# Optimization experiments

Measured on AMD Instinct MI355X. Metric: run time of the kernel, lower is better.

The kernel has to match this reference:

```python
import jax, jax.numpy as jnp
import numpy as np

RADIUS = 1.3
RES = 128
SH_DEG = 2
N_SH = (SH_DEG + 1) ** 2          # 9 SH basis functions
DATA_DIM = N_SH * 3 + 1           # 28: 27 SH rgb coeffs + 1 sigma
STEP = (2.0 * RADIUS / RES) / 2.0 # half a voxel, as in calc_step_size
N_INTRS = int(np.ceil(np.sqrt(3.0) * 2.0 * RES))  # torch.arange(float) length
N_RAYS = 4096


def sh_basis(d):
    # Real spherical harmonics up to degree 2, svox2/plenoxels convention. d: [B,3]
    x, y, z = d[:, 0], d[:, 1], d[:, 2]
    return jnp.stack([
        0.28209479177387814 * jnp.ones_like(x),
        -0.4886025119029199 * y,
        0.4886025119029199 * z,
        -0.4886025119029199 * x,
        1.0925484305920792 * x * y,
        -1.0925484305920792 * y * z,
        0.31539156525252005 * (2.0 * z * z - x * x - y * y),
        -1.0925484305920792 * x * z,
        0.5462742152960396 * (x * x - y * y),
    ], axis=-1)  # [B, 9]


def trilerp(grid, pts):
    # grid: [C, R, R, R] laid out (D,H,W); pts: [N,3] as (x,y,z) in [-1,1],
    # x indexes W, y indexes H, z indexes D (torch grid_sample convention),
    # align_corners=True, padding_mode='border'. Returns [C, N].
    R = grid.shape[-1]
    c = jnp.clip((pts + 1.0) * 0.5 * (R - 1), 0.0, R - 1)  # border padding
    c0 = jnp.floor(c)
    f = c - c0
    i0 = c0.astype(jnp.int32)
    i1 = jnp.minimum(i0 + 1, R - 1)
    x0, y0, z0 = i0[:, 0], i0[:, 1], i0[:, 2]
    x1, y1, z1 = i1[:, 0], i1[:, 1], i1[:, 2]
    fx, fy, fz = f[:, 0], f[:, 1], f[:, 2]
    g = lambda zi, yi, xi: grid[:, zi, yi, xi]  # [C, N]
    out = (g(z0, y0, x0) * ((1 - fz) * (1 - fy) * (1 - fx)) +
           g(z0, y0, x1) * ((1 - fz) * (1 - fy) * fx) +
           g(z0, y1, x0) * ((1 - fz) * fy * (1 - fx)) +
           g(z0, y1, x1) * ((1 - fz) * fy * fx) +
           g(z1, y0, x0) * (fz * (1 - fy) * (1 - fx)) +
           g(z1, y0, x1) * (fz * (1 - fy) * fx) +
           g(z1, y1, x0) * (fz * fy * (1 - fx)) +
           g(z1, y1, x1) * (fz * fy * fx))
    return out


def setup_inputs() -> dict:
    key = jax.random.key(0)
    k1, k2, k3 = jax.random.split(key, 3)
    rays_o = jax.random.normal(k1, (N_RAYS, 3), jnp.float32) * 0.3  # inside cube
    rd = jax.random.normal(k2, (N_RAYS, 3), jnp.float32)
    rays_d = rd / jnp.linalg.norm(rd, axis=-1, keepdims=True)
    # grid parameter: SH coeffs init 0.1, sigma init 0.01 (as in module) + noise
    base = jnp.concatenate([
        jnp.full((1, DATA_DIM - 1, RES, RES, RES), 0.1, jnp.float32),
        jnp.full((1, 1, RES, RES, RES), 0.01, jnp.float32)], axis=1)
    data = base + 0.01 * jax.random.normal(k3, (1, DATA_DIM, RES, RES, RES), jnp.float32)
    return {"rays_o": rays_o, "rays_d": rays_d, "data": data}


def reference(rays_o, rays_d, data):
    # --- ray/box intersection sampling (no grad in original) ---
    ro = jax.lax.stop_gradient(rays_o)
    rd = jax.lax.stop_gradient(rays_d)
    off_pos = (RADIUS - ro) / rd
    off_neg = (-RADIUS - ro) / rd
    start = jnp.max(jnp.minimum(off_pos, off_neg), axis=-1, keepdims=True)  # [B,1]
    steps = jnp.arange(N_INTRS, dtype=ro.dtype)[None, :]
    intersections = start + steps * STEP          # [B, N_INTRS]
    t = intersections[:, :-1]                     # [B, NI]
    pts = ro[:, None, :] + t[..., None] * rd[:, None, :]  # [B, NI, 3]
    mask = jnp.all((pts > -RADIUS) & (pts < RADIUS), axis=-1)  # [B, NI]
    ptsn = pts / RADIUS
    B, NI = t.shape

    # --- trilinear interpolation of grid at all sample points ---
    interp = trilerp(data[0], ptsn.reshape(-1, 3)).T  # [B*NI, 28]
    sigma = jax.nn.relu(interp[:, -1].reshape(B, NI))
    sigma = jnp.where(mask, sigma, 0.0)  # masked_scatter into zeros

    # --- sigma2alpha: standard volumetric compositing weights ---
    dists = (intersections[:, 1:] - intersections[:, :-1]) \
            * jnp.linalg.norm(rays_d, axis=-1, keepdims=True)  # [B, NI]
    alpha = 1.0 - jnp.exp(-sigma * dists)
    trans = jnp.cumprod(jnp.concatenate(
        [jnp.ones((B, 1), alpha.dtype), 1.0 - alpha + 1e-10], axis=1), axis=1)[:, :-1]
    abs_light = alpha * trans  # [B, NI]

    # --- SH -> rgb per sample ---
    sh_mult = sh_basis(rays_d)  # [B, 9]
    sh = interp[:, :-1].reshape(B, NI, 3, N_SH)
    rgb_pts = jnp.einsum('bk,bnck->bnc', sh_mult, sh)  # [B, NI, 3]
    rgb_pts = jnp.where(mask[..., None], rgb_pts, 0.0)  # masked_scatter

    # --- shrgb2rgb: sigmoid, composite, white background ---
    rgb = jnp.sum(abs_light[..., None] * jax.nn.sigmoid(rgb_pts), axis=1)  # [B,3]
    rgb = rgb + (1.0 - jnp.sum(abs_light, axis=1))[..., None]  # white bkgd
    return rgb
```

## Files before the change

kernel.cpp:

```cpp
#include <hip/hip_runtime.h>
#include <math.h>


typedef _Float16 h8 __attribute__((ext_vector_type(8)));

namespace {
constexpr float kRadius   = 1.3f;
constexpr int   kRes      = 128;
constexpr float kStep     = 2.0f * 1.3f / 128.0f / 2.0f;
constexpr int   kNI       = 443;
constexpr int   kNRays    = 4096;
constexpr int   kChStride = kRes * kRes * kRes;
constexpr int   kCh       = 28;
constexpr int   kVoxPad   = 32;
constexpr size_t kVoxBytes = (size_t)kChStride * kVoxPad * sizeof(_Float16);
constexpr int   kChunks   = 2;
constexpr int   kChunks7  = 7;
}

__global__ __launch_bounds__(256)
void convert_grid(const float* __restrict__ grid, _Float16* __restrict__ vox)
{
    const int v = blockIdx.x * 256 + threadIdx.x;
    h8 o[4];
    #pragma unroll
    for (int c = 0; c < kCh; ++c)
        o[c >> 3][c & 7] = (_Float16)__builtin_nontemporal_load(grid + (size_t)c * kChStride + v);
    o[3][4] = o[3][5] = o[3][6] = o[3][7] = (_Float16)0.f;

    h8* dst = (h8*)(vox + (size_t)v * kVoxPad);
    dst[0] = o[0]; dst[1] = o[1]; dst[2] = o[2]; dst[3] = o[3];
}

struct Sample {
    float alpha;
    float a;
    float rp0, rp1, rp2;
    bool  inb;
};

__device__ __forceinline__ Sample eval_sample(
    int k, float start, float ox, float oy, float oz,
    float dx, float dy, float dz, float dist,
    const float* __restrict__ shm, const _Float16* __restrict__ vox)
{
    Sample s;
    s.alpha = 0.f; s.a = 1.f; s.rp0 = s.rp1 = s.rp2 = 0.f; s.inb = false;
    if (k >= kNI) return s;

    const float t  = start + (float)k * kStep;
    const float px = ox + t*dx;
    const float py = oy + t*dy;
    const float pz = oz + t*dz;
    s.inb = (px > -kRadius) && (px < kRadius) &&
            (py > -kRadius) && (py < kRadius) &&
            (pz > -kRadius) && (pz < kRadius);

    float sig = 0.0f;
    if (s.inb) {
        const float cx = fminf(fmaxf((px*(1.0f/kRadius) + 1.0f)*0.5f*127.0f, 0.0f), 127.0f);
        const float cy = fminf(fmaxf((py*(1.0f/kRadius) + 1.0f)*0.5f*127.0f, 0.0f), 127.0f);
        const float cz = fminf(fmaxf((pz*(1.0f/kRadius) + 1.0f)*0.5f*127.0f, 0.0f), 127.0f);
        const float fx0 = floorf(cx), fy0 = floorf(cy), fz0 = floorf(cz);
        const float fx = cx - fx0, fy = cy - fy0, fz = cz - fz0;
        const int ix0 = (int)fx0, iy0 = (int)fy0, iz0 = (int)fz0;
        const int ix1 = min(ix0 + 1, 127);
        const int iy1 = min(iy0 + 1, 127);
        const int iz1 = min(iz0 + 1, 127);

        const float gx0 = 1.0f - fx, gy0 = 1.0f - fy, gz0 = 1.0f - fz;

        const int offs[8] = {
            iz0*(kRes*kRes) + iy0*kRes + ix0,
            iz0*(kRes*kRes) + iy0*kRes + ix1,
            iz0*(kRes*kRes) + iy1*kRes + ix0,
            iz0*(kRes*kRes) + iy1*kRes + ix1,
            iz1*(kRes*kRes) + iy0*kRes + ix0,
            iz1*(kRes*kRes) + iy0*kRes + ix1,
            iz1*(kRes*kRes) + iy1*kRes + ix0,
            iz1*(kRes*kRes) + iy1*kRes + ix1 };
        const float cw[8] = {
            gz0*gy0*gx0, gz0*gy0*fx, gz0*fy*gx0, gz0*fy*fx,
            fz *gy0*gx0, fz *gy0*fx, fz *fy*gx0, fz *fy*fx };

        #pragma unroll
        for (int cn = 0; cn < 8; ++cn) {
            const h8* vp = (const h8*)(vox + (size_t)offs[cn] * kVoxPad);
            const h8 q0 = vp[0], q1 = vp[1], q2 = vp[2], q3 = vp[3];

            float f[28];
            #pragma unroll
            for (int i = 0; i < 8; ++i) f[i]      = (float)q0[i];
            #pragma unroll
            for (int i = 0; i < 8; ++i) f[8 + i]  = (float)q1[i];
            #pragma unroll
            for (int i = 0; i < 8; ++i) f[16 + i] = (float)q2[i];
            #pragma unroll
            for (int i = 0; i < 4; ++i) f[24 + i] = (float)q3[i];

            float r = 0.f, g = 0.f, b = 0.f;
            #pragma unroll
            for (int j = 0; j < 9; ++j) {
                r = fmaf(shm[j], f[j],      r);
                g = fmaf(shm[j], f[9 + j],  g);
                b = fmaf(shm[j], f[18 + j], b);
            }
            const float wc = cw[cn];
            s.rp0 = fmaf(wc, r, s.rp0);
            s.rp1 = fmaf(wc, g, s.rp1);
            s.rp2 = fmaf(wc, b, s.rp2);
            sig   = fmaf(wc, f[27], sig);
        }
        sig = fmaxf(sig, 0.0f);
    }
    s.alpha = 1.0f - expf(-sig * dist);
    s.a     = 1.0f - s.alpha + 1e-10f;
    return s;
}

__device__ __forceinline__ float wave_scan_prod(float a, int lane, float& total)
{
    float prod = a;
    #pragma unroll
    for (int off = 1; off < 64; off <<= 1) {
        const float y = __shfl_up(prod, off, 64);
        if (lane >= off) prod *= y;
    }
    float excl = __shfl_up(prod, 1, 64);
    if (lane == 0) excl = 1.0f;
    total = __shfl(prod, 63, 64);
    return excl;
}

__global__ __launch_bounds__(256, 3)
void render_chunks(const float* __restrict__ rays_o,
                   const float* __restrict__ rays_d,
                   const _Float16* __restrict__ vox,
                   float* __restrict__ partials)
{
    const int lane  = threadIdx.x & 63;
    const int W     = blockIdx.x * 4 + (threadIdx.x >> 6);
    const int ray   = W >> 1;
    const int chunk = W & 1;

    const float ox = rays_o[3*ray+0], oy = rays_o[3*ray+1], oz = rays_o[3*ray+2];
    const float dx = rays_d[3*ray+0], dy = rays_d[3*ray+1], dz = rays_d[3*ray+2];

    const float ppx = ( kRadius - ox)/dx, pnx = (-kRadius - ox)/dx;
    const float ppy = ( kRadius - oy)/dy, pny = (-kRadius - oy)/dy;
    const float ppz = ( kRadius - oz)/dz, pnz = (-kRadius - oz)/dz;
    const float start  = fmaxf(fminf(ppx, pnx), fmaxf(fminf(ppy, pny), fminf(ppz, pnz)));
    const float t_exit = fminf(fmaxf(ppx, pnx), fminf(fmaxf(ppy, pny), fmaxf(ppz, pnz)));

    const int base = chunk * 256;

    if (start + (float)base * kStep > t_exit + kStep) {
        if (lane == 0) {
            float* p = partials + (size_t)(ray * kChunks + chunk) * 5;
            p[0] = 0.f; p[1] = 0.f; p[2] = 0.f; p[3] = 0.f; p[4] = 1.f;
        }
        return;
    }

    const float dnorm = sqrtf(dx*dx + dy*dy + dz*dz);
    const float dist  = kStep * dnorm;

    float shm[9];
    shm[0] =  0.28209479177387814f;
    shm[1] = -0.4886025119029199f * dy;
    shm[2] =  0.4886025119029199f * dz;
    shm[3] = -0.4886025119029199f * dx;
    shm[4] =  1.0925484305920792f * dx * dy;
    shm[5] = -1.0925484305920792f * dy * dz;
    shm[6] =  0.31539156525252005f * (2.0f*dz*dz - dx*dx - dy*dy);
    shm[7] = -1.0925484305920792f * dx * dz;
    shm[8] =  0.5462742152960396f * (dx*dx - dy*dy);

    const Sample A = eval_sample(base       + lane, start, ox, oy, oz, dx, dy, dz, dist, shm, vox);
    const Sample B = eval_sample(base +  64 + lane, start, ox, oy, oz, dx, dy, dz, dist, shm, vox);
    const Sample C = eval_sample(base + 128 + lane, start, ox, oy, oz, dx, dy, dz, dist, shm, vox);
    const Sample D = eval_sample(base + 192 + lane, start, ox, oy, oz, dx, dy, dz, dist, shm, vox);

    float P0, P1, P2, P3;
    const float eA = wave_scan_prod(A.a, lane, P0);
    const float eB = wave_scan_prod(B.a, lane, P1);
    const float eC = wave_scan_prod(C.a, lane, P2);
    const float eD = wave_scan_prod(D.a, lane, P3);

    const float wA = A.alpha * eA;
    const float wB = B.alpha * P0 * eB;
    const float wC = C.alpha * P0 * P1 * eC;
    const float wD = D.alpha * P0 * P1 * P2 * eD;

    float sR = 0.f, sG = 0.f, sB = 0.f;
    if (A.inb) {
        sR = wA * (1.0f / (1.0f + expf(-A.rp0)));
        sG = wA * (1.0f / (1.0f + expf(-A.rp1)));
        sB = wA * (1.0f / (1.0f + expf(-A.rp2)));
    }
    if (B.inb) {
        sR = fmaf(wB, 1.0f / (1.0f + expf(-B.rp0)), sR);
        sG = fmaf(wB, 1.0f / (1.0f + expf(-B.rp1)), sG);
        sB = fmaf(wB, 1.0f / (1.0f + expf(-B.rp2)), sB);
    }
    if (C.inb) {
        sR = fmaf(wC, 1.0f / (1.0f + expf(-C.rp0)), sR);
        sG = fmaf(wC, 1.0f / (1.0f + expf(-C.rp1)), sG);
        sB = fmaf(wC, 1.0f / (1.0f + expf(-C.rp2)), sB);
    }
    if (D.inb) {
        sR = fmaf(wD, 1.0f / (1.0f + expf(-D.rp0)), sR);
        sG = fmaf(wD, 1.0f / (1.0f + expf(-D.rp1)), sG);
        sB = fmaf(wD, 1.0f / (1.0f + expf(-D.rp2)), sB);
    }
    float sL = wA + wB + wC + wD;
    const float P = P0 * P1 * P2 * P3;

    #pragma unroll
    for (int off = 32; off > 0; off >>= 1) {
        sR += __shfl_down(sR, off, 64);
        sG += __shfl_down(sG, off, 64);
        sB += __shfl_down(sB, off, 64);
        sL += __shfl_down(sL, off, 64);
    }

    if (lane == 0) {
        float* p = partials + (size_t)(ray * kChunks + chunk) * 5;
        p[0] = sR; p[1] = sG; p[2] = sB; p[3] = sL; p[4] = P;
    }
}

__global__ __launch_bounds__(256)
void combine_chunks(const float* __restrict__ partials, float* __restrict__ out)
{
    const int r = blockIdx.x * 256 + threadIdx.x;
    const float* p = partials + (size_t)r * (kChunks * 5);

    float carry = 1.0f, aR = 0.f, aG = 0.f, aB = 0.f, aL = 0.f;
    #pragma unroll
    for (int c = 0; c < kChunks; ++c) {
        aR = fmaf(carry, p[c*5 + 0], aR);
        aG = fmaf(carry, p[c*5 + 1], aG);
        aB = fmaf(carry, p[c*5 + 2], aB);
        aL = fmaf(carry, p[c*5 + 3], aL);
        carry *= p[c*5 + 4];
    }
    const float bg = 1.0f - aL;
    out[3*r + 0] = aR + bg;
    out[3*r + 1] = aG + bg;
    out[3*r + 2] = aB + bg;
}

#define TRI8(p) (w000*(p)[o000] + w001*(p)[o001] + w010*(p)[o010] + w011*(p)[o011] \
               + w100*(p)[o100] + w101*(p)[o101] + w110*(p)[o110] + w111*(p)[o111])

__global__ __launch_bounds__(256)
void plenoxel_render_direct(const float* __restrict__ rays_o,
                            const float* __restrict__ rays_d,
                            const float* __restrict__ grid,
                            float* __restrict__ out)
{
    const int lane = threadIdx.x & 63;
    const int ray  = blockIdx.x * 4 + (threadIdx.x >> 6);

    const float ox = rays_o[3*ray+0], oy = rays_o[3*ray+1], oz = rays_o[3*ray+2];
    const float dx = rays_d[3*ray+0], dy = rays_d[3*ray+1], dz = rays_d[3*ray+2];

    const float sx = fminf(( kRadius - ox)/dx, (-kRadius - ox)/dx);
    const float sy = fminf(( kRadius - oy)/dy, (-kRadius - oy)/dy);
    const float sz = fminf(( kRadius - oz)/dz, (-kRadius - oz)/dz);
    const float start = fmaxf(sx, fmaxf(sy, sz));
    const float dnorm = sqrtf(dx*dx + dy*dy + dz*dz);

    float shm[9];
    shm[0] =  0.28209479177387814f;
    shm[1] = -0.4886025119029199f * dy;
    shm[2] =  0.4886025119029199f * dz;
    shm[3] = -0.4886025119029199f * dx;
    shm[4] =  1.0925484305920792f * dx * dy;
    shm[5] = -1.0925484305920792f * dy * dz;
    shm[6] =  0.31539156525252005f * (2.0f*dz*dz - dx*dx - dy*dy);
    shm[7] = -1.0925484305920792f * dx * dz;
    shm[8] =  0.5462742152960396f * (dx*dx - dy*dy);

    float carry = 1.0f;
    float accR = 0.f, accG = 0.f, accB = 0.f, accL = 0.f;

    for (int chunk = 0; chunk < kChunks7; ++chunk) {
        const int k = chunk * 64 + lane;
        float alpha = 0.0f, a = 1.0f;
        float rp0 = 0.f, rp1 = 0.f, rp2 = 0.f;
        bool inb = false;

        if (k < kNI) {
            const float t = start + (float)k * kStep;
            const float dist = kStep * dnorm;
            const float px = ox + t*dx, py = oy + t*dy, pz = oz + t*dz;
            inb = (px > -kRadius) && (px < kRadius) &&
                  (py > -kRadius) && (py < kRadius) &&
                  (pz > -kRadius) && (pz < kRadius);
            float sigma = 0.0f;
            if (inb) {
                const float cx = fminf(fmaxf((px*(1.0f/kRadius) + 1.0f)*0.5f*127.0f, 0.0f), 127.0f);
                const float cy = fminf(fmaxf((py*(1.0f/kRadius) + 1.0f)*0.5f*127.0f, 0.0f), 127.0f);
                const float cz = fminf(fmaxf((pz*(1.0f/kRadius) + 1.0f)*0.5f*127.0f, 0.0f), 127.0f);
                const float fx0 = floorf(cx), fy0 = floorf(cy), fz0 = floorf(cz);
                const float fx = cx - fx0, fy = cy - fy0, fz = cz - fz0;
                const int ix0 = (int)fx0, iy0 = (int)fy0, iz0 = (int)fz0;
                const int ix1 = min(ix0 + 1, 127);
                const int iy1 = min(iy0 + 1, 127);
                const int iz1 = min(iz0 + 1, 127);
                const float gx0 = 1.0f - fx, gy0 = 1.0f - fy, gz0 = 1.0f - fz;
                const float w000 = gz0*gy0*gx0, w001 = gz0*gy0*fx;
                const float w010 = gz0*fy *gx0, w011 = gz0*fy *fx;
                const float w100 = fz *gy0*gx0, w101 = fz *gy0*fx;
                const float w110 = fz *fy *gx0, w111 = fz *fy *fx;
                const int o000 = iz0*(kRes*kRes) + iy0*kRes + ix0;
                const int o001 = iz0*(kRes*kRes) + iy0*kRes + ix1;
                const int o010 = iz0*(kRes*kRes) + iy1*kRes + ix0;
                const int o011 = iz0*(kRes*kRes) + iy1*kRes + ix1;
                const int o100 = iz1*(kRes*kRes) + iy0*kRes + ix0;
                const int o101 = iz1*(kRes*kRes) + iy0*kRes + ix1;
                const int o110 = iz1*(kRes*kRes) + iy1*kRes + ix0;
                const int o111 = iz1*(kRes*kRes) + iy1*kRes + ix1;
                #pragma unroll
                for (int kk = 0; kk < 9; ++kk) {
                    rp0 = fmaf(shm[kk], TRI8(grid + (kk     ) * kChStride), rp0);
                    rp1 = fmaf(shm[kk], TRI8(grid + (kk +  9) * kChStride), rp1);
                    rp2 = fmaf(shm[kk], TRI8(grid + (kk + 18) * kChStride), rp2);
                }
                sigma = fmaxf(TRI8(grid + 27 * kChStride), 0.0f);
            }
            alpha = 1.0f - expf(-sigma * dist);
            a     = 1.0f - alpha + 1e-10f;
        }

        float prod = a;
        #pragma unroll
        for (int off = 1; off < 64; off <<= 1) {
            const float y = __shfl_up(prod, off, 64);
            if (lane >= off) prod *= y;
        }
        float excl = __shfl_up(prod, 1, 64);
        if (lane == 0) excl = 1.0f;
        const float trans = carry * excl;
        const float w = alpha * trans;
        if (inb) {
            accR = fmaf(w, 1.0f / (1.0f + expf(-rp0)), accR);
            accG = fmaf(w, 1.0f / (1.0f + expf(-rp1)), accG);
            accB = fmaf(w, 1.0f / (1.0f + expf(-rp2)), accB);
        }
        accL += w;
        carry *= __shfl(prod, 63, 64);
    }

    #pragma unroll
    for (int off = 32; off > 0; off >>= 1) {
        accR += __shfl_down(accR, off, 64);
        accG += __shfl_down(accG, off, 64);
        accB += __shfl_down(accB, off, 64);
        accL += __shfl_down(accL, off, 64);
    }

    if (lane == 0) {
        const float bg = 1.0f - accL;
        out[3*ray + 0] = accR + bg;
        out[3*ray + 1] = accG + bg;
        out[3*ray + 2] = accB + bg;
    }
}

extern "C" void kernel_launch(void* const* d_in, const int* in_sizes, int n_in,
                              void* d_out, int out_size, void* d_ws, size_t ws_size,
                              hipStream_t stream) {
    const float* rays_o = (const float*)d_in[0];
    const float* rays_d = (const float*)d_in[1];
    const float* data   = (const float*)d_in[2];
    float* out = (float*)d_out;

    const size_t partBytes = (size_t)kNRays * kChunks * 5 * sizeof(float);
    const size_t need = kVoxBytes + partBytes;

    if (ws_size >= need) {
        _Float16* vox = (_Float16*)d_ws;
        float* partials = (float*)((char*)d_ws + kVoxBytes);

        hipLaunchKernelGGL(convert_grid,
                           dim3(kChStride / 256), dim3(256), 0, stream,
                           data, vox);
        hipLaunchKernelGGL(render_chunks,
                           dim3(kNRays * kChunks / 4), dim3(256), 0, stream,
                           rays_o, rays_d, vox, partials);
        hipLaunchKernelGGL(combine_chunks,
                           dim3(kNRays / 256), dim3(256), 0, stream,
                           partials, out);
    } else {
        hipLaunchKernelGGL(plenoxel_render_direct,
                           dim3(kNRays / 4), dim3(256), 0, stream,
                           rays_o, rays_d, data, out);
    }
}
```

Measured before the change: 393.7 us.

## Evaluate adjacent sample pairs per lane and share voxel corner loads

Each lane now handles two consecutive samples along the ray instead of samples 64 apart. When both samples fall in the same voxel cell, the eight corner records are loaded and SH-evaluated once and accumulated with two sets of trilinear weights. This is meant to cut global gathers and SH dot products, since the step is half a voxel and many pairs share a cell. The transmittance scan now runs over per-lane pair products, halving the number of wave scans. In exchange it adds a second, divergent load path for pairs that straddle a cell boundary, and higher register pressure.

```diff
diff --git a/kernel.cpp b/kernel.cpp
--- a/kernel.cpp
+++ b/kernel.cpp
@@ -39,83 +39,167 @@
     bool  inb;
 };
 
-__device__ __forceinline__ Sample eval_sample(
-    int k, float start, float ox, float oy, float oz,
+__device__ __forceinline__ void corner_accum2(
+    const _Float16* __restrict__ rec, const float* __restrict__ shm,
+    float wa, float wb,
+    float& a0, float& a1, float& a2, float& asig,
+    float& b0, float& b1, float& b2, float& bsig)
+{
+    const h8* vp = (const h8*)rec;
+    const h8 q0 = vp[0], q1 = vp[1], q2 = vp[2], q3 = vp[3];
+
+    float f[28];
+    #pragma unroll
+    for (int i = 0; i < 8; ++i) f[i]      = (float)q0[i];
+    #pragma unroll
+    for (int i = 0; i < 8; ++i) f[8 + i]  = (float)q1[i];
+    #pragma unroll
+    for (int i = 0; i < 8; ++i) f[16 + i] = (float)q2[i];
+    #pragma unroll
+    for (int i = 0; i < 4; ++i) f[24 + i] = (float)q3[i];
+
+    float r = 0.f, g = 0.f, b = 0.f;
+    #pragma unroll
+    for (int j = 0; j < 9; ++j) {
+        r = fmaf(shm[j], f[j],      r);
+        g = fmaf(shm[j], f[9 + j],  g);
+        b = fmaf(shm[j], f[18 + j], b);
+    }
+    a0 = fmaf(wa, r, a0);  a1 = fmaf(wa, g, a1);
+    a2 = fmaf(wa, b, a2);  asig = fmaf(wa, f[27], asig);
+    b0 = fmaf(wb, r, b0);  b1 = fmaf(wb, g, b1);
+    b2 = fmaf(wb, b, b2);  bsig = fmaf(wb, f[27], bsig);
+}
+
+__device__ __forceinline__ void corner_accum1(
+    const _Float16* __restrict__ rec, const float* __restrict__ shm,
+    float w, float& a0, float& a1, float& a2, float& asig)
+{
+    const h8* vp = (const h8*)rec;
+    const h8 q0 = vp[0], q1 = vp[1], q2 = vp[2], q3 = vp[3];
+
+    float f[28];
+    #pragma unroll
+    for (int i = 0; i < 8; ++i) f[i]      = (float)q0[i];
+    #pragma unroll
+    for (int i = 0; i < 8; ++i) f[8 + i]  = (float)q1[i];
+    #pragma unroll
+    for (int i = 0; i < 8; ++i) f[16 + i] = (float)q2[i];
+    #pragma unroll
+    for (int i = 0; i < 4; ++i) f[24 + i] = (float)q3[i];
+
+    float r = 0.f, g = 0.f, b = 0.f;
+    #pragma unroll
+    for (int j = 0; j < 9; ++j) {
+        r = fmaf(shm[j], f[j],      r);
+        g = fmaf(shm[j], f[9 + j],  g);
+        b = fmaf(shm[j], f[18 + j], b);
+    }
+    a0 = fmaf(w, r, a0);  a1 = fmaf(w, g, a1);
+    a2 = fmaf(w, b, a2);  asig = fmaf(w, f[27], asig);
+}
+
+__device__ __forceinline__ void eval_pair(
+    int k0, float start, float ox, float oy, float oz,
     float dx, float dy, float dz, float dist,
-    const float* __restrict__ shm, const _Float16* __restrict__ vox)
-{
-    Sample s;
-    s.alpha = 0.f; s.a = 1.f; s.rp0 = s.rp1 = s.rp2 = 0.f; s.inb = false;
-    if (k >= kNI) return s;
-
-    const float t  = start + (float)k * kStep;
-    const float px = ox + t*dx;
-    const float py = oy + t*dy;
-    const float pz = oz + t*dz;
-    s.inb = (px > -kRadius) && (px < kRadius) &&
-            (py > -kRadius) && (py < kRadius) &&
-            (pz > -kRadius) && (pz < kRadius);
-
-    float sig = 0.0f;
-    if (s.inb) {
-        const float cx = fminf(fmaxf((px*(1.0f/kRadius) + 1.0f)*0.5f*127.0f, 0.0f), 127.0f);
-        const float cy = fminf(fmaxf((py*(1.0f/kRadius) + 1.0f)*0.5f*127.0f, 0.0f), 127.0f);
-        const float cz = fminf(fmaxf((pz*(1.0f/kRadius) + 1.0f)*0.5f*127.0f, 0.0f), 127.0f);
-        const float fx0 = floorf(cx), fy0 = floorf(cy), fz0 = floorf(cz);
-        const float fx = cx - fx0, fy = cy - fy0, fz = cz - fz0;
-        const int ix0 = (int)fx0, iy0 = (int)fy0, iz0 = (int)fz0;
-        const int ix1 = min(ix0 + 1, 127);
-        const int iy1 = min(iy0 + 1, 127);
-        const int iz1 = min(iz0 + 1, 127);
-
-        const float gx0 = 1.0f - fx, gy0 = 1.0f - fy, gz0 = 1.0f - fz;
-
-        const int offs[8] = {
-            iz0*(kRes*kRes) + iy0*kRes + ix0,
-            iz0*(kRes*kRes) + iy0*kRes + ix1,
-            iz0*(kRes*kRes) + iy1*kRes + ix0,
-            iz0*(kRes*kRes) + iy1*kRes + ix1,
-            iz1*(kRes*kRes) + iy0*kRes + ix0,
-            iz1*(kRes*kRes) + iy0*kRes + ix1,
-            iz1*(kRes*kRes) + iy1*kRes + ix0,
+    const float* __restrict__ shm, const _Float16* __restrict__ vox,
+    Sample& s0, Sample& s1)
+{
+    s0.alpha = 0.f; s0.a = 1.f; s0.rp0 = s0.rp1 = s0.rp2 = 0.f; s0.inb = false;
+    s1.alpha = 0.f; s1.a = 1.f; s1.rp0 = s1.rp1 = s1.rp2 = 0.f; s1.inb = false;
+
+    const bool v0 = (k0 < kNI), v1 = (k0 + 1 < kNI);
+    const float t0 = start + (float)k0 * kStep;
+    const float t1 = t0 + kStep;
+
+    const float px0 = ox + t0*dx, py0 = oy + t0*dy, pz0 = oz + t0*dz;
+    const float px1 = ox + t1*dx, py1 = oy + t1*dy, pz1 = oz + t1*dz;
+
+    s0.inb = v0 && (px0 > -kRadius) && (px0 < kRadius) &&
+                   (py0 > -kRadius) && (py0 < kRadius) &&
+                   (pz0 > -kRadius) && (pz0 < kRadius);
+    s1.inb = v1 && (px1 > -kRadius) && (px1 < kRadius) &&
+                   (py1 > -kRadius) && (py1 < kRadius) &&
+                   (pz1 > -kRadius) && (pz1 < kRadius);
+
+    const float cx0 = fminf(fmaxf((px0*(1.0f/kRadius) + 1.0f)*0.5f*127.0f, 0.0f), 127.0f);
+    const float cy0 = fminf(fmaxf((py0*(1.0f/kRadius) + 1.0f)*0.5f*127.0f, 0.0f), 127.0f);
+    const float cz0 = fminf(fmaxf((pz0*(1.0f/kRadius) + 1.0f)*0.5f*127.0f, 0.0f), 127.0f);
+    const float cx1 = fminf(fmaxf((px1*(1.0f/kRadius) + 1.0f)*0.5f*127.0f, 0.0f), 127.0f);
+    const float cy1 = fminf(fmaxf((py1*(1.0f/kRadius) + 1.0f)*0.5f*127.0f, 0.0f), 127.0f);
+    const float cz1 = fminf(fmaxf((pz1*(1.0f/kRadius) + 1.0f)*0.5f*127.0f, 0.0f), 127.0f);
+
+    const int ix = (int)floorf(cx0), iy = (int)floorf(cy0), iz = (int)floorf(cz0);
+    const int jx = (int)floorf(cx1), jy = (int)floorf(cy1), jz = (int)floorf(cz1);
+
+    const bool same = s0.inb && s1.inb && (ix == jx) && (iy == jy) && (iz == jz);
+
+    float sig0 = 0.f, sig1 = 0.f;
+
+    if (s0.inb) {
+        const int ix1 = min(ix + 1, 127), iy1 = min(iy + 1, 127), iz1 = min(iz + 1, 127);
+        const float fx = cx0 - (float)ix, fy = cy0 - (float)iy, fz = cz0 - (float)iz;
+        const float gx = 1.f - fx, gy = 1.f - fy, gz = 1.f - fz;
+
+        const float m  = same ? 1.f : 0.f;
+        const float hx = (cx1 - (float)ix) * m;
+        const float hy = (cy1 - (float)iy) * m;
+        const float hz = (cz1 - (float)iz) * m;
+        const float kx = m - hx, ky = m - hy, kz = m - hz;
+
+        const int o[8] = {
+            iz *(kRes*kRes) + iy *kRes + ix,
+            iz *(kRes*kRes) + iy *kRes + ix1,
+            iz *(kRes*kRes) + iy1*kRes + ix,
+            iz *(kRes*kRes) + iy1*kRes + ix1,
+            iz1*(kRes*kRes) + iy *kRes + ix,
+            iz1*(kRes*kRes) + iy *kRes + ix1,
+            iz1*(kRes*kRes) + iy1*kRes + ix,
             iz1*(kRes*kRes) + iy1*kRes + ix1 };
-        const float cw[8] = {
-            gz0*gy0*gx0, gz0*gy0*fx, gz0*fy*gx0, gz0*fy*fx,
-            fz *gy0*gx0, fz *gy0*fx, fz *fy*gx0, fz *fy*fx };
+        const float wa[8] = {
+            gz*gy*gx, gz*gy*fx, gz*fy*gx, gz*fy*fx,
+            fz*gy*gx, fz*gy*fx, fz*fy*gx, fz*fy*fx };
+        const float wb[8] = {
+            kz*ky*kx, kz*ky*hx, kz*hy*kx, kz*hy*hx,
+            hz*ky*kx, hz*ky*hx, hz*hy*kx, hz*hy*hx };
 
         #pragma unroll
-        for (int cn = 0; cn < 8; ++cn) {
-            const h8* vp = (const h8*)(vox + (size_t)offs[cn] * kVoxPad);
-            const h8 q0 = vp[0], q1 = vp[1], q2 = vp[2], q3 = vp[3];
-
-            float f[28];
-            #pragma unroll
-            for (int i = 0; i < 8; ++i) f[i]      = (float)q0[i];
-            #pragma unroll
-            for (int i = 0; i < 8; ++i) f[8 + i]  = (float)q1[i];
-            #pragma unroll
-            for (int i = 0; i < 8; ++i) f[16 + i] = (float)q2[i];
-            #pragma unroll
-            for (int i = 0; i < 4; ++i) f[24 + i] = (float)q3[i];
-
-            float r = 0.f, g = 0.f, b = 0.f;
-            #pragma unroll
-            for (int j = 0; j < 9; ++j) {
-                r = fmaf(shm[j], f[j],      r);
-                g = fmaf(shm[j], f[9 + j],  g);
-                b = fmaf(shm[j], f[18 + j], b);
-            }
-            const float wc = cw[cn];
-            s.rp0 = fmaf(wc, r, s.rp0);
-            s.rp1 = fmaf(wc, g, s.rp1);
-            s.rp2 = fmaf(wc, b, s.rp2);
-            sig   = fmaf(wc, f[27], sig);
-        }
-        sig = fmaxf(sig, 0.0f);
-    }
-    s.alpha = 1.0f - expf(-sig * dist);
-    s.a     = 1.0f - s.alpha + 1e-10f;
-    return s;
+        for (int c = 0; c < 8; ++c)
+            corner_accum2(vox + (size_t)o[c] * kVoxPad, shm, wa[c], wb[c],
+                          s0.rp0, s0.rp1, s0.rp2, sig0,
+                          s1.rp0, s1.rp1, s1.rp2, sig1);
+    }
+
+    if (s1.inb && !same) {
+        const int jx1 = min(jx + 1, 127), jy1 = min(jy + 1, 127), jz1 = min(jz + 1, 127);
+        const float fx = cx1 - (float)jx, fy = cy1 - (float)jy, fz = cz1 - (float)jz;
+        const float gx = 1.f - fx, gy = 1.f - fy, gz = 1.f - fz;
+
+        const int o[8] = {
+            jz *(kRes*kRes) + jy *kRes + jx,
+            jz *(kRes*kRes) + jy *kRes + jx1,
+            jz *(kRes*kRes) + jy1*kRes + jx,
+            jz *(kRes*kRes) + jy1*kRes + jx1,
+            jz1*(kRes*kRes) + jy *kRes + jx,
+            jz1*(kRes*kRes) + jy *kRes + jx1,
+            jz1*(kRes*kRes) + jy1*kRes + jx,
+            jz1*(kRes*kRes) + jy1*kRes + jx1 };
+        const float w[8] = {
+            gz*gy*gx, gz*gy*fx, gz*fy*gx, gz*fy*fx,
+            fz*gy*gx, fz*gy*fx, fz*fy*gx, fz*fy*fx };
+
+        #pragma unroll
+        for (int c = 0; c < 8; ++c)
+            corner_accum1(vox + (size_t)o[c] * kVoxPad, shm, w[c],
+                          s1.rp0, s1.rp1, s1.rp2, sig1);
+    }
+
+    sig0 = fmaxf(sig0, 0.0f);
+    sig1 = fmaxf(sig1, 0.0f);
+    if (s0.inb) { s0.alpha = 1.0f - expf(-sig0 * dist); }
+    if (s1.inb) { s1.alpha = 1.0f - expf(-sig1 * dist); }
+    if (k0 < kNI)     s0.a = 1.0f - s0.alpha + 1e-10f;
+    if (k0 + 1 < kNI) s1.a = 1.0f - s1.alpha + 1e-10f;
 }
 
 __device__ __forceinline__ float wave_scan_prod(float a, int lane, float& total)
@@ -176,45 +260,42 @@
     shm[7] = -1.0925484305920792f * dx * dz;
     shm[8] =  0.5462742152960396f * (dx*dx - dy*dy);
 
-    const Sample A = eval_sample(base       + lane, start, ox, oy, oz, dx, dy, dz, dist, shm, vox);
-    const Sample B = eval_sample(base +  64 + lane, start, ox, oy, oz, dx, dy, dz, dist, shm, vox);
-    const Sample C = eval_sample(base + 128 + lane, start, ox, oy, oz, dx, dy, dz, dist, shm, vox);
-    const Sample D = eval_sample(base + 192 + lane, start, ox, oy, oz, dx, dy, dz, dist, shm, vox);
-
-    float P0, P1, P2, P3;
-    const float eA = wave_scan_prod(A.a, lane, P0);
-    const float eB = wave_scan_prod(B.a, lane, P1);
-    const float eC = wave_scan_prod(C.a, lane, P2);
-    const float eD = wave_scan_prod(D.a, lane, P3);
-
-    const float wA = A.alpha * eA;
-    const float wB = B.alpha * P0 * eB;
-    const float wC = C.alpha * P0 * P1 * eC;
-    const float wD = D.alpha * P0 * P1 * P2 * eD;
+    Sample s0, s1, s2, s3;
+    eval_pair(base       + 2*lane, start, ox, oy, oz, dx, dy, dz, dist, shm, vox, s0, s1);
+    eval_pair(base + 128 + 2*lane, start, ox, oy, oz, dx, dy, dz, dist, shm, vox, s2, s3);
+
+    float P0, P1;
+    const float e0 = wave_scan_prod(s0.a * s1.a, lane, P0);
+    const float e1 = wave_scan_prod(s2.a * s3.a, lane, P1);
+
+    const float w0 = s0.alpha * e0;
+    const float w1 = s1.alpha * e0 * s0.a;
+    const float w2 = s2.alpha * P0 * e1;
+    const float w3 = s3.alpha * P0 * e1 * s2.a;
 
     float sR = 0.f, sG = 0.f, sB = 0.f;
-    if (A.inb) {
-        sR = wA * (1.0f / (1.0f + expf(-A.rp0)));
-        sG = wA * (1.0f / (1.0f + expf(-A.rp1)));
-        sB = wA * (1.0f / (1.0f + expf(-A.rp2)));
-    }
-    if (B.inb) {
-        sR = fmaf(wB, 1.0f / (1.0f + expf(-B.rp0)), sR);
-        sG = fmaf(wB, 1.0f / (1.0f + expf(-B.rp1)), sG);
-        sB = fmaf(wB, 1.0f / (1.0f + expf(-B.rp2)), sB);
-    }
-    if (C.inb) {
-        sR = fmaf(wC, 1.0f / (1.0f + expf(-C.rp0)), sR);
-        sG = fmaf(wC, 1.0f / (1.0f + expf(-C.rp1)), sG);
-        sB = fmaf(wC, 1.0f / (1.0f + expf(-C.rp2)), sB);
-    }
-    if (D.inb) {
-        sR = fmaf(wD, 1.0f / (1.0f + expf(-D.rp0)), sR);
-        sG = fmaf(wD, 1.0f / (1.0f + expf(-D.rp1)), sG);
-        sB = fmaf(wD, 1.0f / (1.0f + expf(-D.rp2)), sB);
-    }
-    float sL = wA + wB + wC + wD;
-    const float P = P0 * P1 * P2 * P3;
+    if (s0.inb) {
+        sR = fmaf(w0, 1.0f / (1.0f + expf(-s0.rp0)), sR);
+        sG = fmaf(w0, 1.0f / (1.0f + expf(-s0.rp1)), sG);
+        sB = fmaf(w0, 1.0f / (1.0f + expf(-s0.rp2)), sB);
+    }
+    if (s1.inb) {
+        sR = fmaf(w1, 1.0f / (1.0f + expf(-s1.rp0)), sR);
+        sG = fmaf(w1, 1.0f / (1.0f + expf(-s1.rp1)), sG);
+        sB = fmaf(w1, 1.0f / (1.0f + expf(-s1.rp2)), sB);
+    }
+    if (s2.inb) {
+        sR = fmaf(w2, 1.0f / (1.0f + expf(-s2.rp0)), sR);
+        sG = fmaf(w2, 1.0f / (1.0f + expf(-s2.rp1)), sG);
+        sB = fmaf(w2, 1.0f / (1.0f + expf(-s2.rp2)), sB);
+    }
+    if (s3.inb) {
+        sR = fmaf(w3, 1.0f / (1.0f + expf(-s3.rp0)), sR);
+        sG = fmaf(w3, 1.0f / (1.0f + expf(-s3.rp1)), sG);
+        sB = fmaf(w3, 1.0f / (1.0f + expf(-s3.rp2)), sB);
+    }
+    float sL = w0 + w1 + w2 + w3;
+    const float P = P0 * P1;
 
     #pragma unroll
     for (int off = 32; off > 0; off >>= 1) {
```

After: 426.6 us. +8.4%, slower.
